# Kernel optimization log

Hardware: AMD Instinct MI355X
Metric: run time of the kernel (lower is better)

Reference implementation:

```python
import jax, jax.numpy as jnp
import numpy as np

N_EMBEDS = 1024
N_HEADS = 16
HEAD_DIM = N_EMBEDS // N_HEADS
SCALE = HEAD_DIM ** (-0.5)
B, T = 2, 2048


def setup_inputs() -> dict:
    key = jax.random.key(0)
    k1, k2, k3, k4 = jax.random.split(key, 4)
    x = jax.random.normal(k1, (B, T, N_EMBEDS), dtype=jnp.float32)
    # Glorot-uniform-style init like keras Dense defaults (scale irrelevant for correctness)
    w_qkv = jax.random.normal(k2, (N_EMBEDS, 3 * N_EMBEDS), dtype=jnp.float32) * (N_EMBEDS ** -0.5)
    w_proj = jax.random.normal(k3, (N_EMBEDS, N_EMBEDS), dtype=jnp.float32) * (N_EMBEDS ** -0.5)
    b_proj = jnp.zeros((N_EMBEDS,), dtype=jnp.float32)
    return {"x": x, "w_qkv": w_qkv, "w_proj": w_proj, "b_proj": b_proj}


def reference(x, w_qkv, w_proj, b_proj):
    Bc, Tc, D = x.shape
    qkv = x @ w_qkv                                   # [B,T,3D]
    q, k, v = jnp.split(qkv, 3, axis=-1)
    def heads(t):
        return t.reshape(Bc, Tc, N_HEADS, HEAD_DIM).transpose(0, 2, 1, 3)  # [B,H,T,hd]
    q, k, v = heads(q), heads(k), heads(v)
    att = jnp.einsum("bhqd,bhkd->bhqk", q, k) * SCALE  # [B,H,T,T]
    causal = jnp.tril(jnp.ones((Tc, Tc), dtype=bool))[None, None]
    att = jnp.where(causal, att, jnp.float32(-1e9))
    att = jax.nn.softmax(att, axis=-1)
    out = jnp.einsum("bhqk,bhkd->bhqd", att, v)        # [B,H,T,hd]
    out = out.transpose(0, 2, 1, 3).reshape(Bc, Tc, D)
    return out @ w_proj + b_proj
```

## Files before the change

### kernel.cpp

```cpp
#include <hip/hip_runtime.h>
#include <hip/hip_bf16.h>


typedef __bf16 bf16;
typedef float f32x4 __attribute__((ext_vector_type(4)));
typedef float f32x16 __attribute__((ext_vector_type(16)));
typedef bf16 bf16x4 __attribute__((ext_vector_type(4)));
typedef bf16 bf16x8 __attribute__((ext_vector_type(8)));

#define B_ 2
#define T_ 2048
#define D_ 1024
#define H_ 16
#define HD_ 64
#define QSPLIT 9

__device__ __forceinline__ f32x16 mfma32(bf16x8 a, bf16x8 b, f32x16 c) {
    return __builtin_amdgcn_mfma_f32_32x32x16_bf16(a, b, c, 0, 0, 0);
}

__device__ __forceinline__ void gload16(void* l, const void* g) {
    __builtin_amdgcn_global_load_lds(
        (const __attribute__((address_space(1))) unsigned int*)g,
        (__attribute__((address_space(3))) unsigned int*)l, 16, 0, 0);
}

__device__ __forceinline__ f32x16 z16() {
    f32x16 v;
#pragma unroll
    for (int i = 0; i < 16; ++i) v[i] = 0.f;
    return v;
}

__global__ __launch_bounds__(256) void cast_f32_bf16(const float* __restrict__ in,
                                                     bf16* __restrict__ out, int n4) {
    int i = blockIdx.x * 256 + threadIdx.x;
    if (i < n4) {
        float4 v = ((const float4*)in)[i];
        bf16x4 o = { (bf16)v.x, (bf16)v.y, (bf16)v.z, (bf16)v.w };
        ((bf16x4*)out)[i] = o;
    }
}

__global__ __launch_bounds__(256) void cast_transpose(const float* __restrict__ in,
                                                      bf16* __restrict__ out, int R, int C) {
    __shared__ float tile[32][33];
    int cx = blockIdx.x * 32 + threadIdx.x;
    int r0 = blockIdx.y * 32;
#pragma unroll
    for (int j = 0; j < 32; j += 8)
        tile[threadIdx.y + j][threadIdx.x] = in[(size_t)(r0 + threadIdx.y + j) * C + cx];
    __syncthreads();
    int rx = r0 + threadIdx.x;
    int c0 = blockIdx.x * 32;
#pragma unroll
    for (int j = 0; j < 32; j += 8)
        out[(size_t)(c0 + threadIdx.y + j) * R + rx] = (bf16)tile[threadIdx.x][threadIdx.y + j];
}

__global__ __launch_bounds__(256) void transpose_v(const bf16* __restrict__ vb,
                                                   bf16* __restrict__ vt) {
    __shared__ bf16 st[64 * 65];
    const int bh = blockIdx.y;
    const int t0 = blockIdx.x * 64;
    const int tid = threadIdx.x;
#pragma unroll
    for (int c = 0; c < 2; ++c) {
        int cid = tid + c * 256;
        int r = cid >> 3, col = (cid & 7) * 8;
        bf16x8 v = *(const bf16x8*)&vb[((size_t)bh * T_ + t0 + r) * HD_ + col];
#pragma unroll
        for (int j = 0; j < 8; ++j) st[r * 65 + col + j] = v[j];
    }
    __syncthreads();
#pragma unroll
    for (int c = 0; c < 2; ++c) {
        int cid = tid + c * 256;
        int tg = cid & 7, d = cid >> 3;
        bf16x8 o;
#pragma unroll
        for (int j = 0; j < 8; ++j) o[j] = st[(tg * 8 + j) * 65 + d];
        *(bf16x8*)&vt[((size_t)bh * HD_ + d) * T_ + t0 + tg * 8] = o;
    }
}

template <int MW, int NWN, int EPI>
__global__ __launch_bounds__(256) void gemm_k(
    const bf16* __restrict__ A, const bf16* __restrict__ Bt,
    int M, int N, int K,
    bf16* __restrict__ qb, bf16* __restrict__ kb, bf16* __restrict__ vb,
    const float* __restrict__ bias, float* __restrict__ outf) {
    constexpr int BM = 64 * MW;
    constexpr int BN = 64 * NWN;
    __shared__ bf16 sA[BM * 64];
    __shared__ bf16 sB[BN * 64];
    const int tid = threadIdx.x;
    const int wave = tid >> 6, lane = tid & 63;
    const int ln = lane & 31, hi = lane >> 5;
    const int wr = (wave >> 1) * (32 * MW);
    const int wc = (wave & 1) * (32 * NWN);
    const int m0 = blockIdx.x * BM, n0 = blockIdx.y * BN;

    f32x16 acc[MW][NWN];
#pragma unroll
    for (int mi = 0; mi < MW; ++mi)
#pragma unroll
        for (int ni = 0; ni < NWN; ++ni) acc[mi][ni] = z16();

    for (int k0 = 0; k0 < K; k0 += 64) {
        __syncthreads();
#pragma unroll
        for (int j = 0; j < 2 * MW; ++j) {
            int c = tid + 256 * j;
            int r = c >> 3, g = (c & 7) ^ (r & 7);
            gload16(&sA[c * 8], A + (size_t)(m0 + r) * K + k0 + 8 * g);
        }
#pragma unroll
        for (int j = 0; j < 2 * NWN; ++j) {
            int c = tid + 256 * j;
            int r = c >> 3, g = (c & 7) ^ (r & 7);
            gload16(&sB[c * 8], Bt + (size_t)(n0 + r) * K + k0 + 8 * g);
        }
        __syncthreads();
#pragma unroll
        for (int s = 0; s < 4; ++s) {
            bf16x8 av[MW], bv[NWN];
#pragma unroll
            for (int mi = 0; mi < MW; ++mi) {
                int r = wr + mi * 32 + ln;
                av[mi] = *(const bf16x8*)((const char*)sA + r * 128 +
                                          ((((s << 1) | hi) ^ (r & 7)) << 4));
            }
#pragma unroll
            for (int ni = 0; ni < NWN; ++ni) {
                int r = wc + ni * 32 + ln;
                bv[ni] = *(const bf16x8*)((const char*)sB + r * 128 +
                                          ((((s << 1) | hi) ^ (r & 7)) << 4));
            }
#pragma unroll
            for (int mi = 0; mi < MW; ++mi)
#pragma unroll
                for (int ni = 0; ni < NWN; ++ni)
                    acc[mi][ni] = mfma32(av[mi], bv[ni], acc[mi][ni]);
        }
    }

#pragma unroll
    for (int mi = 0; mi < MW; ++mi)
#pragma unroll
        for (int ni = 0; ni < NWN; ++ni)
#pragma unroll
            for (int r = 0; r < 16; ++r) {
                int row = m0 + wr + mi * 32 + (r & 3) + 8 * (r >> 2) + 4 * hi;
                int col = n0 + wc + ni * 32 + ln;
                float v = acc[mi][ni][r];
                if (EPI == 0) {
                    int part = col >> 10, h = (col >> 6) & 15, d = col & 63;
                    int b = row >> 11, t = row & (T_ - 1);
                    size_t idx = ((size_t)(b * H_ + h) * T_ + t) * HD_ + d;
                    bf16* dst = (part == 0) ? qb : (part == 1) ? kb : vb;
                    dst[idx] = (bf16)v;
                } else {
                    outf[(size_t)row * N + col] = v + bias[col];
                }
            }
}

__device__ __forceinline__ bf16x8 kread(const char* base, int row, int s, int hi) {
    int b = (row * 128 + s * 32 + hi * 16) ^ ((row & 7) << 4);
    return *(const bf16x8*)(base + b);
}
__device__ __forceinline__ bf16x8 vread(const char* base, int row, int s, int hi) {
    int sw = (row & 7) << 4;
    int b0 = (row * 128 + s * 32 + hi * 8) ^ sw;
    int b1 = (row * 128 + s * 32 + hi * 8 + 16) ^ sw;
    bf16x4 lo = *(const bf16x4*)(base + b0);
    bf16x4 hi4 = *(const bf16x4*)(base + b1);
    return __builtin_shufflevector(lo, hi4, 0, 1, 2, 3, 4, 5, 6, 7);
}

__global__ __launch_bounds__(256, 3) void attn_kernel(
    const bf16* __restrict__ qb, const bf16* __restrict__ kb,
    const bf16* __restrict__ vtb, bf16* __restrict__ ob,
    bf16* __restrict__ oP, float2* __restrict__ mlP) {
    __shared__ bf16 sK2[2][4096];
    __shared__ bf16 sV2[2][4096];

    const int bid = blockIdx.x;
    const int bh = bid & 31;
    const int sid = bid >> 5;
    int qt, seg, t0, t1;
    if (sid < QSPLIT) {
        qt = sid; seg = -1; t0 = 0; t1 = 2 * qt + 2;
    } else {
        int idx = sid - QSPLIT;
        qt = QSPLIT + (idx >> 1);
        seg = idx & 1;
        if (seg == 0) { t0 = 0; t1 = qt + 1; }
        else          { t0 = qt + 1; t1 = 2 * qt + 2; }
    }
    const int b = bh >> 4, h = bh & 15;
    const int tid = threadIdx.x, wave = tid >> 6, lane = tid & 63;
    const int ln = lane & 31, hi = lane >> 5;
    const int qs = qt * 128 + wave * 32;
    const int qrow = qs + ln;

    const bf16* Qg = qb + (size_t)bh * (T_ * HD_);
    const bf16* Kg = kb + (size_t)bh * (T_ * HD_);
    const bf16* Vtg = vtb + (size_t)bh * (HD_ * T_);

    bf16x8 qf[4];
#pragma unroll
    for (int s = 0; s < 4; ++s) {
        bf16x8 v = *(const bf16x8*)&Qg[(size_t)qrow * HD_ + s * 16 + hi * 8];
#pragma unroll
        for (int e = 0; e < 8; ++e) v[e] = (bf16)((float)v[e] * 0.1803368801f);
        qf[s] = v;
    }

    const int rr0 = tid >> 3;
    const int gg = ((tid & 7) ^ (rr0 & 7)) * 8;

    {
        int kv0 = t0 * 64;
        gload16(&sK2[0][tid * 8], Kg + (size_t)(kv0 + rr0) * HD_ + gg);
        gload16(&sK2[0][(tid + 256) * 8], Kg + (size_t)(kv0 + rr0 + 32) * HD_ + gg);
        gload16(&sV2[0][tid * 8], Vtg + (size_t)rr0 * T_ + kv0 + gg);
        gload16(&sV2[0][(tid + 256) * 8], Vtg + (size_t)(rr0 + 32) * T_ + kv0 + gg);
    }
    __syncthreads();

    const float NINF = -__builtin_inff();
    f32x16 oA = z16(), oB = z16();
    float mR = NINF, lR = 0.f;
    int cur = 0;

    for (int t = t0; t < t1; ++t) {
        if ((t + 1) < t1) {
            int kv0 = (t + 1) * 64;
            bf16* kd = sK2[cur ^ 1];
            bf16* vd = sV2[cur ^ 1];
            gload16(&kd[tid * 8], Kg + (size_t)(kv0 + rr0) * HD_ + gg);
            gload16(&kd[(tid + 256) * 8], Kg + (size_t)(kv0 + rr0 + 32) * HD_ + gg);
            gload16(&vd[tid * 8], Vtg + (size_t)rr0 * T_ + kv0 + gg);
            gload16(&vd[(tid + 256) * 8], Vtg + (size_t)(rr0 + 32) * T_ + kv0 + gg);
        }

        if (64 * t <= qs + 31) {
            const char* kbase = (const char*)sK2[cur];
            const char* vbase = (const char*)sV2[cur];

            f32x16 p0 = z16(), p1 = z16();
            __builtin_amdgcn_s_setprio(1);
#pragma unroll
            for (int s = 0; s < 4; ++s) {
                bf16x8 a0 = kread(kbase, ln, s, hi);
                bf16x8 a1 = kread(kbase, ln + 32, s, hi);
                p0 = mfma32(a0, qf[s], p0);
                p1 = mfma32(a1, qf[s], p1);
            }
            __builtin_amdgcn_s_setprio(0);

            if (64 * t + 63 > qs) {
                int kvb = 64 * t + 4 * hi;
#pragma unroll
                for (int r = 0; r < 16; ++r) {
                    int kvr = kvb + (r & 3) + 8 * (r >> 2);
                    if (kvr > qrow) p0[r] = NINF;
                    if (kvr + 32 > qrow) p1[r] = NINF;
                }
            }

            float mx0 = NINF, mx1 = NINF, mx2 = NINF, mx3 = NINF;
#pragma unroll
            for (int r = 0; r < 16; r += 4) {
                mx0 = fmaxf(mx0, p0[r]);     mx1 = fmaxf(mx1, p0[r + 1]);
                mx2 = fmaxf(mx2, p0[r + 2]); mx3 = fmaxf(mx3, p0[r + 3]);
                mx0 = fmaxf(mx0, p1[r]);     mx1 = fmaxf(mx1, p1[r + 1]);
                mx2 = fmaxf(mx2, p1[r + 2]); mx3 = fmaxf(mx3, p1[r + 3]);
            }
            float pm = fmaxf(fmaxf(mx0, mx1), fmaxf(mx2, mx3));
            pm = fmaxf(pm, __shfl_xor(pm, 32));

            if (__any(pm > mR + 8.f)) {
                float mnew = fmaxf(mR, pm);
                float fac = exp2f(mR - mnew);
                lR *= fac;
#pragma unroll
                for (int r = 0; r < 16; ++r) { oA[r] *= fac; oB[r] *= fac; }
                mR = mnew;
            }

            float s0 = 0.f, s1 = 0.f, s2 = 0.f, s3 = 0.f;
            bf16x8 pa0, pa1, pa2, pa3;
#pragma unroll
            for (int e = 0; e < 8; ++e) {
                float a = exp2f(p0[e] - mR);      s0 += a;  pa0[e] = (bf16)a;
                float bb = exp2f(p0[8 + e] - mR); s1 += bb; pa1[e] = (bf16)bb;
                float c = exp2f(p1[e] - mR);      s2 += c;  pa2[e] = (bf16)c;
                float d = exp2f(p1[8 + e] - mR);  s3 += d;  pa3[e] = (bf16)d;
            }
            float rs = (s0 + s1) + (s2 + s3);
            rs += __shfl_xor(rs, 32);
            lR += rs;

            __builtin_amdgcn_s_setprio(1);
#pragma unroll
            for (int s = 0; s < 4; ++s) {
                bf16x8 pas = (s == 0) ? pa0 : (s == 1) ? pa1 : (s == 2) ? pa2 : pa3;
                oA = mfma32(vread(vbase, ln, s, hi), pas, oA);
                oB = mfma32(vread(vbase, ln + 32, s, hi), pas, oB);
            }
            __builtin_amdgcn_s_setprio(0);
        }

        __syncthreads();
        cur ^= 1;
    }

    if (seg < 0) {
        float inv = 1.f / lR;
        bf16* orow = ob + ((size_t)(b * T_ + qrow)) * D_ + h * HD_;
#pragma unroll
        for (int g = 0; g < 4; ++g) {
            bf16x4 w, w2;
#pragma unroll
            for (int j = 0; j < 4; ++j) {
                w[j] = (bf16)(oA[4 * g + j] * inv);
                w2[j] = (bf16)(oB[4 * g + j] * inv);
            }
            *(bf16x4*)&orow[4 * hi + 8 * g] = w;
            *(bf16x4*)&orow[32 + 4 * hi + 8 * g] = w2;
        }
    } else {
        int row = wave * 32 + ln;
        size_t sbase = (((size_t)bh * (16 - QSPLIT) + (qt - QSPLIT)) * 2 + seg);
        bf16* prow = oP + (sbase * 128 + row) * 64;
#pragma unroll
        for (int g = 0; g < 4; ++g) {
            bf16x4 w, w2;
#pragma unroll
            for (int j = 0; j < 4; ++j) {
                w[j] = (bf16)oA[4 * g + j];
                w2[j] = (bf16)oB[4 * g + j];
            }
            *(bf16x4*)&prow[4 * hi + 8 * g] = w;
            *(bf16x4*)&prow[32 + 4 * hi + 8 * g] = w2;
        }
        if (hi == 0) mlP[sbase * 128 + row] = make_float2(mR, lR);
    }
}

__global__ __launch_bounds__(256) void attn_merge(
    const bf16* __restrict__ oP, const float2* __restrict__ mlP,
    bf16* __restrict__ ob) {
    constexpr int NQS = 16 - QSPLIT;
    int gid = blockIdx.x * 256 + threadIdx.x;
    int bh = gid / (NQS * 128);
    int rem = gid - bh * (NQS * 128);
    int qi = rem >> 7, row = rem & 127;
    int b = bh >> 4, h = bh & 15;
    int t = (QSPLIT + qi) * 128 + row;
    size_t sbase = ((size_t)bh * NQS + qi) * 2;
    float2 ml0 = mlP[(sbase + 0) * 128 + row];
    float2 ml1 = mlP[(sbase + 1) * 128 + row];
    float ms = fmaxf(ml0.x, ml1.x);
    float w0 = exp2f(ml0.x - ms), w1 = exp2f(ml1.x - ms);
    float inv = 1.f / (ml0.y * w0 + ml1.y * w1);
    w0 *= inv; w1 *= inv;
    const bf16* r0 = oP + ((sbase + 0) * 128 + row) * 64;
    const bf16* r1 = oP + ((sbase + 1) * 128 + row) * 64;
    bf16* dst = ob + ((size_t)(b * T_ + t)) * D_ + h * HD_;
#pragma unroll
    for (int g = 0; g < 8; ++g) {
        bf16x8 a = *(const bf16x8*)&r0[g * 8];
        bf16x8 c = *(const bf16x8*)&r1[g * 8];
        bf16x8 o;
#pragma unroll
        for (int j = 0; j < 8; ++j)
            o[j] = (bf16)((float)a[j] * w0 + (float)c[j] * w1);
        *(bf16x8*)&dst[g * 8] = o;
    }
}

extern "C" void kernel_launch(void* const* d_in, const int* in_sizes, int n_in,
                              void* d_out, int out_size, void* d_ws, size_t ws_size,
                              hipStream_t stream) {
    const float* x = (const float*)d_in[0];
    const float* w_qkv = (const float*)d_in[1];
    const float* w_proj = (const float*)d_in[2];
    const float* b_proj = (const float*)d_in[3];
    float* out = (float*)d_out;
    char* ws = (char*)d_ws;

    bf16* xb = (bf16*)(ws);
    bf16* ob = (bf16*)(ws);
    bf16* wqkvt = (bf16*)(ws + 8388608);
    bf16* vtbuf = (bf16*)(ws + 8388608);
    bf16* qbuf = (bf16*)(ws + 16777216);
    bf16* wprojt = (bf16*)(ws + 16777216);
    bf16* kbuf = (bf16*)(ws + 25165824);
    bf16* vbuf = (bf16*)(ws + 33554432);
    bf16* oP = (bf16*)(ws + 33554432);
    float2* mlP = (float2*)(ws + 33554432 + 7340032);

    cast_f32_bf16<<<4096, 256, 0, stream>>>(x, xb, (B_ * T_ * D_) / 4);
    dim3 tb(32, 8);
    cast_transpose<<<dim3(3 * D_ / 32, D_ / 32), tb, 0, stream>>>(w_qkv, wqkvt, D_, 3 * D_);

    gemm_k<2, 2, 0><<<dim3((B_ * T_) / 128, (3 * D_) / 128), 256, 0, stream>>>(
        xb, wqkvt, B_ * T_, 3 * D_, D_, qbuf, kbuf, vbuf, nullptr, nullptr);

    transpose_v<<<dim3(T_ / 64, B_ * H_), 256, 0, stream>>>(vbuf, vtbuf);

    attn_kernel<<<23 * 32, 256, 0, stream>>>(qbuf, kbuf, vtbuf, ob, oP, mlP);
    attn_merge<<<112, 256, 0, stream>>>(oP, mlP, ob);

    cast_transpose<<<dim3(D_ / 32, D_ / 32), tb, 0, stream>>>(w_proj, wprojt, D_, D_);

    gemm_k<1, 2, 1><<<dim3((B_ * T_) / 64, D_ / 128), 256, 0, stream>>>(
        ob, wprojt, B_ * T_, D_, D_, nullptr, nullptr, nullptr, b_proj, out);
}
```

Before: 124.8 us.

## Generalize attention KV split to variable segments per query tile, MFMA row sums

Replaces the fixed two-way KV split for late query tiles with a variable number of segments (up to four) per query tile, sized to balance work across 34 blocks per batch-head. The merge kernel now combines up to four partial outputs per row. The row-sum reduction of softmax probabilities moves from VALU adds plus a cross-lane shuffle into an extra set of MFMAs against a ones vector. Launch bounds are raised to 4 blocks per CU, and the partial output buffer is moved into the output tensor to free workspace. The extra MFMAs and larger merge traffic add work in exchange for better load balance and occupancy.

```diff
diff --git a/kernel.cpp b/kernel.cpp
--- a/kernel.cpp
+++ b/kernel.cpp
@@ -13,7 +13,8 @@
 #define D_ 1024
 #define H_ 16
 #define HD_ 64
-#define QSPLIT 9
+#define SEGS_PER_BH 34
+#define SPLIT_PER_BH 29
 
 __device__ __forceinline__ f32x16 mfma32(bf16x8 a, bf16x8 b, f32x16 c) {
     return __builtin_amdgcn_mfma_f32_32x32x16_bf16(a, b, c, 0, 0, 0);
@@ -179,7 +180,7 @@
     return __builtin_shufflevector(lo, hi4, 0, 1, 2, 3, 4, 5, 6, 7);
 }
 
-__global__ __launch_bounds__(256, 3) void attn_kernel(
+__global__ __launch_bounds__(256, 4) void attn_kernel(
     const bf16* __restrict__ qb, const bf16* __restrict__ kb,
     const bf16* __restrict__ vtb, bf16* __restrict__ ob,
     bf16* __restrict__ oP, float2* __restrict__ mlP) {
@@ -187,18 +188,22 @@
     __shared__ bf16 sV2[2][4096];
 
     const int bid = blockIdx.x;
-    const int bh = bid & 31;
-    const int sid = bid >> 5;
-    int qt, seg, t0, t1;
-    if (sid < QSPLIT) {
-        qt = sid; seg = -1; t0 = 0; t1 = 2 * qt + 2;
-    } else {
-        int idx = sid - QSPLIT;
-        qt = QSPLIT + (idx >> 1);
-        seg = idx & 1;
-        if (seg == 0) { t0 = 0; t1 = qt + 1; }
-        else          { t0 = qt + 1; t1 = 2 * qt + 2; }
-    }
+    const int bh = bid / SEGS_PER_BH;
+    int u = bid - bh * SEGS_PER_BH;
+    int qt = 0, ps = 0, ns;
+    for (;;) {
+        ns = (2 * qt + 11) / 10;
+        if (u < ns) break;
+        if (qt >= 5) ps += ns;
+        u -= ns;
+        ++qt;
+    }
+    const int seg = u;
+    const int nt = 2 * qt + 2;
+    const int len = (nt + ns - 1) / ns;
+    const int t0 = seg * len;
+    const int t1 = (t0 + len < nt) ? (t0 + len) : nt;
+
     const int b = bh >> 4, h = bh & 15;
     const int tid = threadIdx.x, wave = tid >> 6, lane = tid & 63;
     const int ln = lane & 31, hi = lane >> 5;
@@ -217,6 +222,10 @@
         for (int e = 0; e < 8; ++e) v[e] = (bf16)((float)v[e] * 0.1803368801f);
         qf[s] = v;
     }
+
+    bf16x8 ones;
+#pragma unroll
+    for (int e = 0; e < 8; ++e) ones[e] = (bf16)1.0f;
 
     const int rr0 = tid >> 3;
     const int gg = ((tid & 7) ^ (rr0 & 7)) * 8;
@@ -274,10 +283,10 @@
             float mx0 = NINF, mx1 = NINF, mx2 = NINF, mx3 = NINF;
 #pragma unroll
             for (int r = 0; r < 16; r += 4) {
-                mx0 = fmaxf(mx0, p0[r]);     mx1 = fmaxf(mx1, p0[r + 1]);
-                mx2 = fmaxf(mx2, p0[r + 2]); mx3 = fmaxf(mx3, p0[r + 3]);
-                mx0 = fmaxf(mx0, p1[r]);     mx1 = fmaxf(mx1, p1[r + 1]);
-                mx2 = fmaxf(mx2, p1[r + 2]); mx3 = fmaxf(mx3, p1[r + 3]);
+                mx0 = fmaxf(fmaxf(p0[r], p1[r]), mx0);
+                mx1 = fmaxf(fmaxf(p0[r + 1], p1[r + 1]), mx1);
+                mx2 = fmaxf(fmaxf(p0[r + 2], p1[r + 2]), mx2);
+                mx3 = fmaxf(fmaxf(p0[r + 3], p1[r + 3]), mx3);
             }
             float pm = fmaxf(fmaxf(mx0, mx1), fmaxf(mx2, mx3));
             pm = fmaxf(pm, __shfl_xor(pm, 32));
@@ -291,20 +300,20 @@
                 mR = mnew;
             }
 
-            float s0 = 0.f, s1 = 0.f, s2 = 0.f, s3 = 0.f;
             bf16x8 pa0, pa1, pa2, pa3;
 #pragma unroll
             for (int e = 0; e < 8; ++e) {
-                float a = exp2f(p0[e] - mR);      s0 += a;  pa0[e] = (bf16)a;
-                float bb = exp2f(p0[8 + e] - mR); s1 += bb; pa1[e] = (bf16)bb;
-                float c = exp2f(p1[e] - mR);      s2 += c;  pa2[e] = (bf16)c;
-                float d = exp2f(p1[8 + e] - mR);  s3 += d;  pa3[e] = (bf16)d;
-            }
-            float rs = (s0 + s1) + (s2 + s3);
-            rs += __shfl_xor(rs, 32);
-            lR += rs;
+                pa0[e] = (bf16)exp2f(p0[e] - mR);
+                pa1[e] = (bf16)exp2f(p0[8 + e] - mR);
+                pa2[e] = (bf16)exp2f(p1[e] - mR);
+                pa3[e] = (bf16)exp2f(p1[8 + e] - mR);
+            }
 
             __builtin_amdgcn_s_setprio(1);
+            f32x16 sacc = mfma32(ones, pa0, z16());
+            sacc = mfma32(ones, pa1, sacc);
+            sacc = mfma32(ones, pa2, sacc);
+            sacc = mfma32(ones, pa3, sacc);
 #pragma unroll
             for (int s = 0; s < 4; ++s) {
                 bf16x8 pas = (s == 0) ? pa0 : (s == 1) ? pa1 : (s == 2) ? pa2 : pa3;
@@ -312,13 +321,14 @@
                 oB = mfma32(vread(vbase, ln + 32, s, hi), pas, oB);
             }
             __builtin_amdgcn_s_setprio(0);
+            lR += sacc[0];
         }
 
         __syncthreads();
         cur ^= 1;
     }
 
-    if (seg < 0) {
+    if (ns == 1) {
         float inv = 1.f / lR;
         bf16* orow = ob + ((size_t)(b * T_ + qrow)) * D_ + h * HD_;
 #pragma unroll
@@ -334,8 +344,8 @@
         }
     } else {
         int row = wave * 32 + ln;
-        size_t sbase = (((size_t)bh * (16 - QSPLIT) + (qt - QSPLIT)) * 2 + seg);
-        bf16* prow = oP + (sbase * 128 + row) * 64;
+        size_t sidx = (size_t)bh * SPLIT_PER_BH + ps + seg;
+        bf16* prow = oP + (sidx * 128 + row) * 64;
 #pragma unroll
         for (int g = 0; g < 4; ++g) {
             bf16x4 w, w2;
@@ -347,38 +357,57 @@
             *(bf16x4*)&prow[4 * hi + 8 * g] = w;
             *(bf16x4*)&prow[32 + 4 * hi + 8 * g] = w2;
         }
-        if (hi == 0) mlP[sbase * 128 + row] = make_float2(mR, lR);
+        if (hi == 0) mlP[sidx * 128 + row] = make_float2(mR, lR);
     }
 }
 
 __global__ __launch_bounds__(256) void attn_merge(
     const bf16* __restrict__ oP, const float2* __restrict__ mlP,
     bf16* __restrict__ ob) {
-    constexpr int NQS = 16 - QSPLIT;
     int gid = blockIdx.x * 256 + threadIdx.x;
-    int bh = gid / (NQS * 128);
-    int rem = gid - bh * (NQS * 128);
+    int bh = gid / (11 * 128);
+    int rem = gid - bh * (11 * 128);
     int qi = rem >> 7, row = rem & 127;
+    int qt = qi + 5;
+    int ns = (2 * qt + 11) / 10;
+    int ps = 0;
+    for (int q = 5; q < qt; ++q) ps += (2 * q + 11) / 10;
+    size_t sb = (size_t)bh * SPLIT_PER_BH + ps;
     int b = bh >> 4, h = bh & 15;
-    int t = (QSPLIT + qi) * 128 + row;
-    size_t sbase = ((size_t)bh * NQS + qi) * 2;
-    float2 ml0 = mlP[(sbase + 0) * 128 + row];
-    float2 ml1 = mlP[(sbase + 1) * 128 + row];
-    float ms = fmaxf(ml0.x, ml1.x);
-    float w0 = exp2f(ml0.x - ms), w1 = exp2f(ml1.x - ms);
-    float inv = 1.f / (ml0.y * w0 + ml1.y * w1);
-    w0 *= inv; w1 *= inv;
-    const bf16* r0 = oP + ((sbase + 0) * 128 + row) * 64;
-    const bf16* r1 = oP + ((sbase + 1) * 128 + row) * 64;
+    int t = qt * 128 + row;
+
+    float2 mls[4];
+    float mx = -__builtin_inff();
+#pragma unroll
+    for (int s = 0; s < 4; ++s)
+        if (s < ns) {
+            mls[s] = mlP[(sb + s) * 128 + row];
+            mx = fmaxf(mx, mls[s].x);
+        }
+    float w[4];
+    float den = 0.f;
+#pragma unroll
+    for (int s = 0; s < 4; ++s)
+        if (s < ns) {
+            w[s] = exp2f(mls[s].x - mx);
+            den += w[s] * mls[s].y;
+        }
+    float inv = 1.f / den;
+
     bf16* dst = ob + ((size_t)(b * T_ + t)) * D_ + h * HD_;
 #pragma unroll
     for (int g = 0; g < 8; ++g) {
-        bf16x8 a = *(const bf16x8*)&r0[g * 8];
-        bf16x8 c = *(const bf16x8*)&r1[g * 8];
+        float acc[8] = {0.f, 0.f, 0.f, 0.f, 0.f, 0.f, 0.f, 0.f};
+#pragma unroll
+        for (int s = 0; s < 4; ++s)
+            if (s < ns) {
+                bf16x8 v = *(const bf16x8*)&oP[((sb + s) * 128 + row) * 64 + g * 8];
+#pragma unroll
+                for (int j = 0; j < 8; ++j) acc[j] += w[s] * (float)v[j];
+            }
         bf16x8 o;
 #pragma unroll
-        for (int j = 0; j < 8; ++j)
-            o[j] = (bf16)((float)a[j] * w0 + (float)c[j] * w1);
+        for (int j = 0; j < 8; ++j) o[j] = (bf16)(acc[j] * inv);
         *(bf16x8*)&dst[g * 8] = o;
     }
 }
@@ -401,8 +430,8 @@
     bf16* wprojt = (bf16*)(ws + 16777216);
     bf16* kbuf = (bf16*)(ws + 25165824);
     bf16* vbuf = (bf16*)(ws + 33554432);
-    bf16* oP = (bf16*)(ws + 33554432);
-    float2* mlP = (float2*)(ws + 33554432 + 7340032);
+    float2* mlP = (float2*)(ws + 33554432);
+    bf16* oP = (bf16*)d_out;
 
     cast_f32_bf16<<<4096, 256, 0, stream>>>(x, xb, (B_ * T_ * D_) / 4);
     dim3 tb(32, 8);
@@ -413,8 +442,8 @@
 
     transpose_v<<<dim3(T_ / 64, B_ * H_), 256, 0, stream>>>(vbuf, vtbuf);
 
-    attn_kernel<<<23 * 32, 256, 0, stream>>>(qbuf, kbuf, vtbuf, ob, oP, mlP);
-    attn_merge<<<112, 256, 0, stream>>>(oP, mlP, ob);
+    attn_kernel<<<SEGS_PER_BH * 32, 256, 0, stream>>>(qbuf, kbuf, vtbuf, ob, oP, mlP);
+    attn_merge<<<176, 256, 0, stream>>>(oP, mlP, ob);
 
     cast_transpose<<<dim3(D_ / 32, D_ / 32), tb, 0, stream>>>(w_proj, wprojt, D_, D_);
 
```

Result: slower. 140.4 us (+12.5%).

## Triple-buffer K/V tiles, software-pipeline QK^T one step ahead, compute row sums via MFMA

Applied to the files above, without the earlier changes.

Moves from double to triple LDS buffering so the K/V tiles two steps ahead are prefetched. The QK^T MFMAs for the next tile are issued before the current tile's softmax and PV, so matrix work can overlap the exp/max vector work. Row-sum accumulation switches from VALU adds plus a cross-lane shuffle to extra MFMAs against a ones vector, summing the bf16-rounded probabilities. LDS use grows by half and register pressure rises from the extra score accumulators, which may hurt occupancy at the requested three blocks per CU.

```diff
diff --git a/kernel.cpp b/kernel.cpp
--- a/kernel.cpp
+++ b/kernel.cpp
@@ -183,8 +183,8 @@
     const bf16* __restrict__ qb, const bf16* __restrict__ kb,
     const bf16* __restrict__ vtb, bf16* __restrict__ ob,
     bf16* __restrict__ oP, float2* __restrict__ mlP) {
-    __shared__ bf16 sK2[2][4096];
-    __shared__ bf16 sV2[2][4096];
+    __shared__ bf16 sK3[3][4096];
+    __shared__ bf16 sV3[3][4096];
 
     const int bid = blockIdx.x;
     const int bh = bid & 31;
@@ -217,67 +217,67 @@
         for (int e = 0; e < 8; ++e) v[e] = (bf16)((float)v[e] * 0.1803368801f);
         qf[s] = v;
     }
+    bf16x8 ones;
+#pragma unroll
+    for (int e = 0; e < 8; ++e) ones[e] = (bf16)1.0f;
 
     const int rr0 = tid >> 3;
     const int gg = ((tid & 7) ^ (rr0 & 7)) * 8;
 
-    {
-        int kv0 = t0 * 64;
-        gload16(&sK2[0][tid * 8], Kg + (size_t)(kv0 + rr0) * HD_ + gg);
-        gload16(&sK2[0][(tid + 256) * 8], Kg + (size_t)(kv0 + rr0 + 32) * HD_ + gg);
-        gload16(&sV2[0][tid * 8], Vtg + (size_t)rr0 * T_ + kv0 + gg);
-        gload16(&sV2[0][(tid + 256) * 8], Vtg + (size_t)(rr0 + 32) * T_ + kv0 + gg);
-    }
+    auto stage = [&](int t, int buf) {
+        int kv0 = t * 64;
+        gload16(&sK3[buf][tid * 8], Kg + (size_t)(kv0 + rr0) * HD_ + gg);
+        gload16(&sK3[buf][(tid + 256) * 8], Kg + (size_t)(kv0 + rr0 + 32) * HD_ + gg);
+        gload16(&sV3[buf][tid * 8], Vtg + (size_t)rr0 * T_ + kv0 + gg);
+        gload16(&sV3[buf][(tid + 256) * 8], Vtg + (size_t)(rr0 + 32) * T_ + kv0 + gg);
+    };
+    auto qk = [&](int buf, f32x16& q0, f32x16& q1) {
+        const char* kbase = (const char*)sK3[buf];
+        q0 = z16(); q1 = z16();
+        __builtin_amdgcn_s_setprio(1);
+#pragma unroll
+        for (int s = 0; s < 4; ++s) {
+            q0 = mfma32(kread(kbase, ln, s, hi), qf[s], q0);
+            q1 = mfma32(kread(kbase, ln + 32, s, hi), qf[s], q1);
+        }
+        __builtin_amdgcn_s_setprio(0);
+    };
+
+    stage(t0, 0);
+    __syncthreads();
+    if (t0 + 1 < t1) stage(t0 + 1, 1);
+    f32x16 pA0, pA1, pB0, pB1;
+    qk(0, pA0, pA1);
     __syncthreads();
 
     const float NINF = -__builtin_inff();
     f32x16 oA = z16(), oB = z16();
     float mR = NINF, lR = 0.f;
-    int cur = 0;
-
-    for (int t = t0; t < t1; ++t) {
-        if ((t + 1) < t1) {
-            int kv0 = (t + 1) * 64;
-            bf16* kd = sK2[cur ^ 1];
-            bf16* vd = sV2[cur ^ 1];
-            gload16(&kd[tid * 8], Kg + (size_t)(kv0 + rr0) * HD_ + gg);
-            gload16(&kd[(tid + 256) * 8], Kg + (size_t)(kv0 + rr0 + 32) * HD_ + gg);
-            gload16(&vd[tid * 8], Vtg + (size_t)rr0 * T_ + kv0 + gg);
-            gload16(&vd[(tid + 256) * 8], Vtg + (size_t)(rr0 + 32) * T_ + kv0 + gg);
-        }
+    int c = 0;
+
+    auto step = [&](int t, f32x16& pc0, f32x16& pc1, f32x16& pn0, f32x16& pn1) {
+        const int bn = (c + 1 == 3) ? 0 : c + 1;
+        const int b2 = (bn + 1 == 3) ? 0 : bn + 1;
+        if (t + 2 < t1) stage(t + 2, b2);
+        if (t + 1 < t1 && 64 * (t + 1) <= qs + 31) qk(bn, pn0, pn1);
 
         if (64 * t <= qs + 31) {
-            const char* kbase = (const char*)sK2[cur];
-            const char* vbase = (const char*)sV2[cur];
-
-            f32x16 p0 = z16(), p1 = z16();
-            __builtin_amdgcn_s_setprio(1);
-#pragma unroll
-            for (int s = 0; s < 4; ++s) {
-                bf16x8 a0 = kread(kbase, ln, s, hi);
-                bf16x8 a1 = kread(kbase, ln + 32, s, hi);
-                p0 = mfma32(a0, qf[s], p0);
-                p1 = mfma32(a1, qf[s], p1);
-            }
-            __builtin_amdgcn_s_setprio(0);
-
             if (64 * t + 63 > qs) {
                 int kvb = 64 * t + 4 * hi;
 #pragma unroll
                 for (int r = 0; r < 16; ++r) {
                     int kvr = kvb + (r & 3) + 8 * (r >> 2);
-                    if (kvr > qrow) p0[r] = NINF;
-                    if (kvr + 32 > qrow) p1[r] = NINF;
+                    if (kvr > qrow) pc0[r] = NINF;
+                    if (kvr + 32 > qrow) pc1[r] = NINF;
                 }
             }
-
             float mx0 = NINF, mx1 = NINF, mx2 = NINF, mx3 = NINF;
 #pragma unroll
             for (int r = 0; r < 16; r += 4) {
-                mx0 = fmaxf(mx0, p0[r]);     mx1 = fmaxf(mx1, p0[r + 1]);
-                mx2 = fmaxf(mx2, p0[r + 2]); mx3 = fmaxf(mx3, p0[r + 3]);
-                mx0 = fmaxf(mx0, p1[r]);     mx1 = fmaxf(mx1, p1[r + 1]);
-                mx2 = fmaxf(mx2, p1[r + 2]); mx3 = fmaxf(mx3, p1[r + 3]);
+                mx0 = fmaxf(fmaxf(pc0[r], pc1[r]), mx0);
+                mx1 = fmaxf(fmaxf(pc0[r + 1], pc1[r + 1]), mx1);
+                mx2 = fmaxf(fmaxf(pc0[r + 2], pc1[r + 2]), mx2);
+                mx3 = fmaxf(fmaxf(pc0[r + 3], pc1[r + 3]), mx3);
             }
             float pm = fmaxf(fmaxf(mx0, mx1), fmaxf(mx2, mx3));
             pm = fmaxf(pm, __shfl_xor(pm, 32));
@@ -291,20 +291,21 @@
                 mR = mnew;
             }
 
-            float s0 = 0.f, s1 = 0.f, s2 = 0.f, s3 = 0.f;
             bf16x8 pa0, pa1, pa2, pa3;
 #pragma unroll
             for (int e = 0; e < 8; ++e) {
-                float a = exp2f(p0[e] - mR);      s0 += a;  pa0[e] = (bf16)a;
-                float bb = exp2f(p0[8 + e] - mR); s1 += bb; pa1[e] = (bf16)bb;
-                float c = exp2f(p1[e] - mR);      s2 += c;  pa2[e] = (bf16)c;
-                float d = exp2f(p1[8 + e] - mR);  s3 += d;  pa3[e] = (bf16)d;
-            }
-            float rs = (s0 + s1) + (s2 + s3);
-            rs += __shfl_xor(rs, 32);
-            lR += rs;
-
+                pa0[e] = (bf16)exp2f(pc0[e] - mR);
+                pa1[e] = (bf16)exp2f(pc0[8 + e] - mR);
+                pa2[e] = (bf16)exp2f(pc1[e] - mR);
+                pa3[e] = (bf16)exp2f(pc1[8 + e] - mR);
+            }
+
+            const char* vbase = (const char*)sV3[c];
             __builtin_amdgcn_s_setprio(1);
+            f32x16 sacc = mfma32(ones, pa0, z16());
+            sacc = mfma32(ones, pa1, sacc);
+            sacc = mfma32(ones, pa2, sacc);
+            sacc = mfma32(ones, pa3, sacc);
 #pragma unroll
             for (int s = 0; s < 4; ++s) {
                 bf16x8 pas = (s == 0) ? pa0 : (s == 1) ? pa1 : (s == 2) ? pa2 : pa3;
@@ -312,10 +313,16 @@
                 oB = mfma32(vread(vbase, ln + 32, s, hi), pas, oB);
             }
             __builtin_amdgcn_s_setprio(0);
+            lR += sacc[0];
         }
 
         __syncthreads();
-        cur ^= 1;
+        c = bn;
+    };
+
+    for (int t = t0; t < t1; t += 2) {
+        step(t, pA0, pA1, pB0, pB1);
+        if (t + 1 < t1) step(t + 1, pB0, pB1, pA0, pA1);
     }
 
     if (seg < 0) {
```

Result: slower. 328.2 us (+162.9%).
